# Performance work log

Hardware: AMD Instinct MI355X
Metric: run time of the kernel (lower is better)

## Reference

```python
import jax, jax.numpy as jnp
import numpy as np

V_SIZE, E, H = 30000, 256, 128   # vocab, emb_dim, GRU hidden per direction
B, U, T, ND = 32, 32, 128, 64    # dialogues, utterances, max tokens, dialogue-id table size
SCALE = E ** 0.5                  # attention normalise_factor = hid_size**0.5, hid_size = emb_dim


def _gru_dir(x_seq, w_ih, w_hh, b_ih, b_hh):
    """Unidirectional torch-style GRU. x_seq: [N,T,E] -> [N,T,H]."""
    xp = jnp.einsum('nte,ge->ntg', x_seq, w_ih) + b_ih   # precompute input gates [N,T,3H]
    xp = jnp.swapaxes(xp, 0, 1)                          # [T,N,3H]

    def step(h, xpt):
        gh = h @ w_hh.T + b_hh
        r = jax.nn.sigmoid(xpt[:, :H] + gh[:, :H])
        z = jax.nn.sigmoid(xpt[:, H:2 * H] + gh[:, H:2 * H])
        n = jnp.tanh(xpt[:, 2 * H:] + r * gh[:, 2 * H:])
        h_new = (1.0 - z) * n + z * h
        return h_new, h_new

    h0 = jnp.zeros((x_seq.shape[0], H), x_seq.dtype)
    _, out = jax.lax.scan(step, h0, xp)
    return jnp.swapaxes(out, 0, 1)


def _forward(x, d_ids, utt_len, emb_table,
             w_ih_f, w_hh_f, b_ih_f, b_hh_f,
             w_ih_b, w_hh_b, b_ih_b, b_hh_b,
             wq, bq, wk, bk, wv, bv, wo, bo, wl, bl):
    b, u, t = x.shape
    N = b * u
    emb = emb_table[x.reshape(N, t)]                      # [N,T,E]
    lens = jnp.clip(utt_len[d_ids].reshape(N), 1, t)      # valid tokens per utterance
    pos = jnp.arange(t)
    # index map that reverses the valid prefix (padding region clipped, unused)
    rev_idx = jnp.clip(lens[:, None] - 1 - pos[None, :], 0, t - 1)  # [N,T]

    o_f = _gru_dir(emb, w_ih_f, w_hh_f, b_ih_f, b_hh_f)   # causal => correct on valid prefix
    emb_rev = jnp.take_along_axis(emb, rev_idx[:, :, None], axis=1)
    o_b = jnp.take_along_axis(_gru_dir(emb_rev, w_ih_b, w_hh_b, b_ih_b, b_hh_b),
                              rev_idx[:, :, None], axis=1)
    h = jnp.concatenate([o_f, o_b], axis=-1)              # [N,T,E] bi-GRU states

    # self-attention pooling; original takes op[-1], so only the query at the
    # last valid token (lens-1) is needed -- identical math, less compute.
    k = jnp.einsum('nte,he->nth', h, wk) + bk
    v = jnp.einsum('nte,he->nth', h, wv) + bv
    h_last = jnp.take_along_axis(h, (lens - 1)[:, None, None], axis=1)[:, 0]  # [N,E]
    q = h_last @ wq.T + bq
    score = jnp.einsum('nh,nth->nt', q, k) / SCALE
    score = jnp.where(pos[None, :] < lens[:, None], score, -jnp.inf)
    attn = jax.nn.softmax(score, axis=-1)
    ctx = jnp.einsum('nt,nth->nh', attn, v)
    out = (ctx @ wo.T + bo) @ wl.T + bl                   # make_output then final linear
    return out.reshape(b, u, -1)


def setup_inputs() -> dict:
    key = jax.random.key(0)
    ks = jax.random.split(key, 16)

    def p(k, shape):
        return (jax.random.normal(k, shape, jnp.float32) / np.sqrt(shape[-1])).astype(jnp.float32)

    return {
        'x': jax.random.randint(ks[0], (B, U, T), 0, V_SIZE, dtype=jnp.int32),
        'd_ids': jax.random.randint(ks[1], (B,), 0, ND, dtype=jnp.int32),
        'utt_len': jax.random.randint(ks[2], (ND, U), 1, T + 1, dtype=jnp.int32),
        'emb_table': p(ks[3], (V_SIZE, E)),
        'w_ih_f': p(ks[4], (3 * H, E)), 'w_hh_f': p(ks[5], (3 * H, H)),
        'b_ih_f': jnp.zeros(3 * H, jnp.float32), 'b_hh_f': jnp.zeros(3 * H, jnp.float32),
        'w_ih_b': p(ks[6], (3 * H, E)), 'w_hh_b': p(ks[7], (3 * H, H)),
        'b_ih_b': jnp.zeros(3 * H, jnp.float32), 'b_hh_b': jnp.zeros(3 * H, jnp.float32),
        'wq': p(ks[8], (E, E)), 'bq': jnp.zeros(E, jnp.float32),
        'wk': p(ks[9], (E, E)), 'bk': jnp.zeros(E, jnp.float32),
        'wv': p(ks[10], (E, E)), 'bv': jnp.zeros(E, jnp.float32),
        'wo': p(ks[11], (E, E)), 'bo': jnp.zeros(E, jnp.float32),
        'wl': p(ks[12], (E, E)), 'bl': jnp.zeros(E, jnp.float32),
    }


def reference(x, d_ids, utt_len, emb_table,
              w_ih_f, w_hh_f, b_ih_f, b_hh_f,
              w_ih_b, w_hh_b, b_ih_b, b_hh_b,
              wq, bq, wk, bk, wv, bv, wo, bo, wl, bl):
    return _forward(x, d_ids, utt_len, emb_table,
                    w_ih_f, w_hh_f, b_ih_f, b_hh_f,
                    w_ih_b, w_hh_b, b_ih_b, b_hh_b,
                    wq, bq, wk, bk, wv, bv, wo, bo, wl, bl)
```

## Files before the change

### kernel.cpp

```cpp
#include <hip/hip_runtime.h>
#include <hip/hip_bf16.h>
#include <math.h>
#include <stdint.h>

typedef unsigned short u16;
typedef unsigned int   u32;
typedef __attribute__((ext_vector_type(8))) short bf16x8;
typedef __attribute__((ext_vector_type(4))) float f32x4;

#define EDIM 256
#define HDIM 128
#define TLEN 128
#define NUTT 1024
#define UU   32
#define NBU  8

#define WS_FLAG 0
#define WS_COPY 8192
#define WS_EMB  1048576LL
#define WS_OF   18874368LL
#define WS_OB   52428800LL

#define MFMA16(a, b, c) __builtin_amdgcn_mfma_f32_16x16x32_bf16((a), (b), (c), 0, 0, 0)
#define SOUT(u, s, j) ((u) * 1096 + (s) * 136 + (j))

__device__ __forceinline__ float b2f(u16 b) {
    u32 u = ((u32)b) << 16; float f; __builtin_memcpy(&f, &u, 4); return f;
}
__device__ __forceinline__ u16 f2b(float f) {
    u32 u; __builtin_memcpy(&u, &f, 4);
    u32 r = u + 0x7FFFu + ((u >> 16) & 1u);
    return (u16)(r >> 16);
}
__device__ __forceinline__ u16 f2b_hw(float f) {
    __hip_bfloat16 h = __float2bfloat16(f);
    u16 v; __builtin_memcpy(&v, &h, 2); return v;
}
__device__ __forceinline__ float fsigmoid(float x) { return 1.0f / (1.0f + __expf(-x)); }
__device__ __forceinline__ float ftanh(float x) { return 1.0f - 2.0f / (__expf(2.0f * x) + 1.0f); }

__device__ __forceinline__ bf16x8 ldw8(const void* p, size_t off, int flag) {
    if (flag) {
        const float* f = (const float*)p + off;
        float4 a = *(const float4*)f;
        float4 b = *(const float4*)(f + 4);
        union { u16 e[8]; bf16x8 v; } r;
        r.e[0] = f2b_hw(a.x); r.e[1] = f2b_hw(a.y);
        r.e[2] = f2b_hw(a.z); r.e[3] = f2b_hw(a.w);
        r.e[4] = f2b_hw(b.x); r.e[5] = f2b_hw(b.y);
        r.e[6] = f2b_hw(b.z); r.e[7] = f2b_hw(b.w);
        return r.v;
    }
    return *(const bf16x8*)((const u16*)p + off);
}
__device__ __forceinline__ float ldb(const void* p, int i, int flag) {
    return flag ? ((const float*)p)[i] : b2f(((const u16*)p)[i]);
}

__global__ __launch_bounds__(256)
void k_convert(void* ws, const void* emb, const void* wq, const void* wk,
               const void* wv, const void* wo, const void* wl) {
    __shared__ int scnt[4];
    const int tid = threadIdx.x, lane = tid & 63, wid = tid >> 6;
    const u16* p = (const u16*)emb;
    int cnt = 0;
#pragma unroll 8
    for (int i = tid; i < 16384; i += 256)
        cnt += ((p[i] & 0x7F80) == 0x7F80) ? 1 : 0;
#pragma unroll
    for (int o = 32; o > 0; o >>= 1) cnt += __shfl_down(cnt, o);
    if (lane == 0) scnt[wid] = cnt;
    __syncthreads();
    const int flag = (scnt[0] + scnt[1] + scnt[2] + scnt[3] > 0) ? 1 : 0;
    if (blockIdx.x == 0 && tid == 0) *(int*)((char*)ws + WS_FLAG) = flag;

    const void* mats[5] = {wq, wk, wv, wo, wl};
    u16* base = (u16*)((char*)ws + WS_COPY);
    const int gtid = blockIdx.x * 256 + tid;
    const int gs   = gridDim.x * 256;
    for (int q = gtid; q < 5 * 16384; q += gs) {
        const int mi = q >> 14;
        const int g  = q & 16383;
        const int e4 = g * 4;
        const int rowa = e4 >> 8, colb = e4 & 255;
        u16 e[4];
        if (flag) {
            float4 v = ((const float4*)mats[mi])[g];
            e[0] = f2b(v.x); e[1] = f2b(v.y); e[2] = f2b(v.z); e[3] = f2b(v.w);
        } else {
            uint2 v = ((const uint2*)mats[mi])[g];
            e[0] = (u16)v.x; e[1] = (u16)(v.x >> 16);
            e[2] = (u16)v.y; e[3] = (u16)(v.y >> 16);
        }
        u16* dst = base + mi * 65536;
        if (mi == 1) {
            u16* dd = dst + (rowa >> 3) * 2048 + colb * 8 + (rowa & 7);
            dd[0] = e[0]; dd[8] = e[1]; dd[16] = e[2]; dd[24] = e[3];
        } else {
            u16* dd = dst + (colb >> 3) * 2048 + rowa * 8 + (colb & 7);
            dd[0] = e[0]; dd[1] = e[1]; dd[2] = e[2]; dd[3] = e[3];
        }
    }

    if (flag == 0) return;
    {
        const float4* src = (const float4*)emb;
        uint2* dst = (uint2*)((char*)ws + WS_EMB);
        for (int i = gtid; i < 1920000; i += gs) {
            float4 v = src[i];
            uint2 pk;
            pk.x = (u32)f2b(v.x) | ((u32)f2b(v.y) << 16);
            pk.y = (u32)f2b(v.z) | ((u32)f2b(v.w) << 16);
            dst[i] = pk;
        }
    }
}

__global__ __launch_bounds__(512)
void k_scan(const int* __restrict__ x, void* ws,
            const int* __restrict__ d_ids, const int* __restrict__ utt_len,
            const void* embp,
            const void* wihf, const void* whhf, const void* bihf, const void* bhhf,
            const void* wihb, const void* whhb, const void* bihb, const void* bhhb) {
    const int dir = blockIdx.y;
    const void* w_ih = dir ? wihb : wihf;
    const void* w_hh = dir ? whhb : whhf;
    const void* b_ih = dir ? bihb : bihf;
    const void* b_hh = dir ? bhhb : bhhf;
    u16* outp = (u16*)((char*)ws + (dir ? WS_OB : WS_OF));
    const int flag = *(const int*)((const char*)ws + WS_FLAG);
    const u16* emb = flag ? (const u16*)((char*)ws + WS_EMB) : (const u16*)embp;

    const int n0 = blockIdx.x * NBU;
    __shared__ __align__(16) u16 sh_emb[2][NBU][264];
    __shared__ __align__(16) u16 sh_hi[2][NBU * 136];
    __shared__ __align__(16) u16 sh_lo[2][NBU * 136];
    __shared__ __align__(16) u16 sh_out[2][NBU * 1096];
    __shared__ int sh_tok[NBU * 132];
    __shared__ int sh_L[NBU];

    const int tid = threadIdx.x, lane = tid & 63, wvi = tid >> 6;
    const int q4 = lane >> 4, mm = lane & 15;
    const int j = wvi * 16 + mm;
    const int u8 = mm & 7;
    const int arr0 = (q4 & 2);
    const bool a2 = (arr0 != 0);
    const bool lo32 = (lane < 32);

    for (int i = tid; i < NBU * 136; i += 512) { sh_hi[0][i] = 0; sh_lo[0][i] = 0; }
    for (int i = tid; i < NBU * TLEN; i += 512) {
        const int u = i >> 7, tt = i & 127;
        sh_tok[u * 132 + tt] = x[(n0 + u) * TLEN + tt];
    }
    if (tid < NBU) {
        const int gn = n0 + tid;
        const int L = utt_len[d_ids[gn >> 5] * UU + (gn & 31)];
        sh_L[tid] = min(max(L, 1), TLEN);
    }

    bf16x8 wih[3][8]; bf16x8 whh[3][4];
    float bcr, bcz, bxn, bgn;
#pragma unroll
    for (int n3 = 0; n3 < 3; ++n3) {
        const int g = n3 * HDIM + j;
#pragma unroll
        for (int ks = 0; ks < 8; ++ks)
            wih[n3][ks] = ldw8(w_ih, (size_t)g * EDIM + ks * 32 + q4 * 8, flag);
#pragma unroll
        for (int ks = 0; ks < 4; ++ks)
            whh[n3][ks] = ldw8(w_hh, (size_t)g * HDIM + ks * 32 + q4 * 8, flag);
    }
    bcr = ldb(b_ih, j, flag) + ldb(b_hh, j, flag);
    bcz = ldb(b_ih, HDIM + j, flag) + ldb(b_hh, HDIM + j, flag);
    bxn = ldb(b_ih, 2 * HDIM + j, flag);
    bgn = ldb(b_hh, 2 * HDIM + j, flag);

    float hprev[2] = {0.f, 0.f};
    const f32x4 zero4 = {0.f, 0.f, 0.f, 0.f};
    __syncthreads();

    int Lm = sh_L[0];
#pragma unroll
    for (int u = 1; u < NBU; ++u) Lm = max(Lm, sh_L[u]);
    const int tmax = (Lm + 7) & ~7;

    const int pf_u = lane & 7;
    const int pf_c = (wvi & 3) * 8 + (lane >> 3);
    const int pf_L = sh_L[pf_u];
    const int tsel = wvi >> 2;

    {
        const int te = dir ? max(pf_L - 1 - tsel, 0) : tsel;
        const int tok = sh_tok[pf_u * 132 + te];
        uint4 v = *(const uint4*)(emb + (size_t)tok * EDIM + pf_c * 8);
        *(uint4*)&sh_emb[tsel][pf_u][pf_c * 8] = v;
    }
    __syncthreads();

    for (int t0 = 0; t0 < tmax; t0 += 2) {
        const int obuf = (t0 >> 3) & 1;
        const bool more = (t0 + 2 < tmax);

        uint4 pf;
        if (more) {
            const int tt = t0 + 2 + tsel;
            const int te = dir ? max(pf_L - 1 - tt, 0) : tt;
            const int tok = sh_tok[pf_u * 132 + te];
            pf = *(const uint4*)(emb + (size_t)tok * EDIM + pf_c * 8);
        }

        f32x4 accx[3];
        {
            const u16* eb_ = (mm < 8) ? &sh_emb[0][u8][0] : &sh_emb[1][u8][0];
            bf16x8 a = *(const bf16x8*)(eb_ + q4 * 8);
            accx[0] = MFMA16(a, wih[0][0], zero4);
            accx[1] = MFMA16(a, wih[1][0], zero4);
            accx[2] = MFMA16(a, wih[2][0], zero4);
#pragma unroll
            for (int ks = 1; ks < 8; ++ks) {
                bf16x8 av = *(const bf16x8*)(eb_ + ks * 32 + q4 * 8);
                accx[0] = MFMA16(av, wih[0][ks], accx[0]);
                accx[1] = MFMA16(av, wih[1][ks], accx[1]);
                accx[2] = MFMA16(av, wih[2][ks], accx[2]);
            }
        }
        float xA[3][2], xB[3][2];
#pragma unroll
        for (int g = 0; g < 3; ++g) {
#pragma unroll
            for (int r = 0; r < 2; ++r) {
                const float sv = a2 ? accx[g][r] : accx[g][2 + r];
                const float ov = a2 ? accx[g][2 + r] : accx[g][r];
                const float pv = __shfl_xor(sv, 32);
                xA[g][r] = lo32 ? ov : pv;
                xB[g][r] = lo32 ? pv : ov;
            }
        }

        {
            f32x4 accg[3];
            const u16* hb_ = ((mm < 8) ? sh_hi[0] : sh_lo[0]) + u8 * 136;
            {
                bf16x8 a = *(const bf16x8*)(hb_ + q4 * 8);
                accg[0] = MFMA16(a, whh[0][0], zero4);
                accg[1] = MFMA16(a, whh[1][0], zero4);
                accg[2] = MFMA16(a, whh[2][0], zero4);
            }
#pragma unroll
            for (int ks = 1; ks < 4; ++ks) {
                bf16x8 a = *(const bf16x8*)(hb_ + ks * 32 + q4 * 8);
                accg[0] = MFMA16(a, whh[0][ks], accg[0]);
                accg[1] = MFMA16(a, whh[1][ks], accg[1]);
                accg[2] = MFMA16(a, whh[2][ks], accg[2]);
            }
            const int slot = t0 & 7;
#pragma unroll
            for (int r = 0; r < 2; ++r) {
                float gg[3];
#pragma unroll
                for (int g = 0; g < 3; ++g) {
                    const float sv = a2 ? accg[g][r] : accg[g][2 + r];
                    const float ov = a2 ? accg[g][2 + r] : accg[g][r];
                    gg[g] = ov + __shfl_xor(sv, 32);
                }
                const int u = (q4 * 4 + arr0 + r) & 7;
                const float rg = fsigmoid(xA[0][r] + gg[0] + bcr);
                const float zg = fsigmoid(xA[1][r] + gg[1] + bcz);
                const float nn = ftanh((xA[2][r] + bxn) + rg * (gg[2] + bgn));
                const float hn = (1.0f - zg) * nn + zg * hprev[r];
                hprev[r] = hn;
                const u16 hb16 = f2b_hw(hn);
                sh_hi[1][u * 136 + j] = hb16;
                sh_lo[1][u * 136 + j] = f2b_hw(hn - b2f(hb16));
                sh_out[obuf][SOUT(u, slot, j)] = hb16;
            }
        }
        __syncthreads();

        {
            f32x4 accg[3];
            const u16* hb_ = ((mm < 8) ? sh_hi[1] : sh_lo[1]) + u8 * 136;
            {
                bf16x8 a = *(const bf16x8*)(hb_ + q4 * 8);
                accg[0] = MFMA16(a, whh[0][0], zero4);
                accg[1] = MFMA16(a, whh[1][0], zero4);
                accg[2] = MFMA16(a, whh[2][0], zero4);
            }
#pragma unroll
            for (int ks = 1; ks < 4; ++ks) {
                bf16x8 a = *(const bf16x8*)(hb_ + ks * 32 + q4 * 8);
                accg[0] = MFMA16(a, whh[0][ks], accg[0]);
                accg[1] = MFMA16(a, whh[1][ks], accg[1]);
                accg[2] = MFMA16(a, whh[2][ks], accg[2]);
            }
            const int slot = (t0 & 7) + 1;
#pragma unroll
            for (int r = 0; r < 2; ++r) {
                float gg[3];
#pragma unroll
                for (int g = 0; g < 3; ++g) {
                    const float sv = a2 ? accg[g][r] : accg[g][2 + r];
                    const float ov = a2 ? accg[g][2 + r] : accg[g][r];
                    gg[g] = ov + __shfl_xor(sv, 32);
                }
                const int u = (q4 * 4 + arr0 + r) & 7;
                const float rg = fsigmoid(xB[0][r] + gg[0] + bcr);
                const float zg = fsigmoid(xB[1][r] + gg[1] + bcz);
                const float nn = ftanh((xB[2][r] + bxn) + rg * (gg[2] + bgn));
                const float hn = (1.0f - zg) * nn + zg * hprev[r];
                hprev[r] = hn;
                const u16 hb16 = f2b_hw(hn);
                sh_hi[0][u * 136 + j] = hb16;
                sh_lo[0][u * 136 + j] = f2b_hw(hn - b2f(hb16));
                sh_out[obuf][SOUT(u, slot, j)] = hb16;
            }
        }
        if (more)
            *(uint4*)&sh_emb[tsel][pf_u][pf_c * 8] = pf;
        __syncthreads();

        if (((t0 + 1) & 7) == 7) {
            const int rowIdx = tid >> 3;
            const int part   = tid & 7;
            const int fu = rowIdx >> 3, fs = rowIdx & 7;
            const int tt = ((t0 + 1) & ~7) + fs;
            const int tout = dir ? (sh_L[fu] - 1 - tt) : tt;
            if (tout >= 0) {
                const u16* srcp = &sh_out[obuf][SOUT(fu, fs, part * 16)];
                uint4 v0 = *(const uint4*)(srcp);
                uint4 v1 = *(const uint4*)(srcp + 8);
                u16* dstp = outp + ((size_t)(n0 + fu) * TLEN + tout) * HDIM + part * 16;
                *(uint4*)(dstp)     = v0;
                *(uint4*)(dstp + 8) = v1;
            }
        }
    }
}

__device__ __forceinline__ float matvec_tiled(const u16* __restrict__ wt,
                                              const float* __restrict__ vin,
                                              int tid, float bias) {
    float s0 = bias, s1 = 0.0f;
#pragma unroll
    for (int kt = 0; kt < 32; kt += 2) {
        bf16x8 w8 = *(const bf16x8*)(wt + kt * 2048 + tid * 8);
        bf16x8 w9 = *(const bf16x8*)(wt + (kt + 1) * 2048 + tid * 8);
#pragma unroll
        for (int d = 0; d < 8; ++d) {
            s0 += b2f((u16)w8[d]) * vin[kt * 8 + d];
            s1 += b2f((u16)w9[d]) * vin[kt * 8 + 8 + d];
        }
    }
    return s0 + s1;
}

__global__ __launch_bounds__(256)
void k_attn(void* ws, void* outv,
            const int* __restrict__ d_ids, const int* __restrict__ utt_len,
            const void* bqp, const void* bvp, const void* bop, const void* blp) {
    const u16* wt = (const u16*)((char*)ws + WS_COPY);
    const u16* wq = wt;
    const u16* wk = wt + 65536;
    const u16* wv = wt + 2 * 65536;
    const u16* wo = wt + 3 * 65536;
    const u16* wl = wt + 4 * 65536;
    const int flag = *(const int*)((const char*)ws + WS_FLAG);

    const int n = blockIdx.x;
    const int L = min(max(utt_len[d_ids[n >> 5] * UU + (n & 31)], 1), TLEN);
    const u16* hf = (const u16*)((char*)ws + WS_OF) + (size_t)n * TLEN * HDIM;
    const u16* hb = (const u16*)((char*)ws + WS_OB) + (size_t)n * TLEN * HDIM;

    __shared__ float sh_hl[EDIM];
    __shared__ float sh_v1[EDIM];
    __shared__ float sh_uv[EDIM];
    __shared__ float sh_a[4 * EDIM];
    __shared__ float sh_m[4], sh_l[4];

    const int tid = threadIdx.x, lane = tid & 63, wid = tid >> 6;

    sh_hl[tid] = (tid < HDIM) ? b2f(hf[(size_t)(L - 1) * HDIM + tid])
                              : b2f(hb[(size_t)(L - 1) * HDIM + (tid - HDIM)]);
    __syncthreads();

    sh_v1[tid] = matvec_tiled(wq, sh_hl, tid, ldb(bqp, tid, flag));
    __syncthreads();

    sh_uv[tid] = matvec_tiled(wk, sh_v1, tid, 0.0f);
    __syncthreads();

    {
        const int e0 = lane * 4;
        const float u0 = sh_uv[e0], u1 = sh_uv[e0 + 1];
        const float u2 = sh_uv[e0 + 2], u3 = sh_uv[e0 + 3];
        float m = -1e30f, l = 0.0f;
        float a0 = 0.f, a1 = 0.f, a2 = 0.f, a3 = 0.f;
        const size_t lofs = (lane < 32) ? (size_t)(lane * 4)
                                        : (size_t)((lane - 32) * 4);
        const u16* hbase = (lane < 32) ? hf : hb;
        for (int t = wid; t < L; t += 8) {
            const int tB = t + 4;
            const int tBc = (tB < L) ? tB : (L - 1);
            uint2 pvA = *(const uint2*)(hbase + (size_t)t * HDIM + lofs);
            uint2 pvB = *(const uint2*)(hbase + (size_t)tBc * HDIM + lofs);
            const float hA0 = b2f((u16)(pvA.x & 0xFFFF));
            const float hA1 = b2f((u16)(pvA.x >> 16));
            const float hA2 = b2f((u16)(pvA.y & 0xFFFF));
            const float hA3 = b2f((u16)(pvA.y >> 16));
            const float hB0 = b2f((u16)(pvB.x & 0xFFFF));
            const float hB1 = b2f((u16)(pvB.x >> 16));
            const float hB2 = b2f((u16)(pvB.y & 0xFFFF));
            const float hB3 = b2f((u16)(pvB.y >> 16));
            float pA = hA0 * u0 + hA1 * u1 + hA2 * u2 + hA3 * u3;
            float pB = hB0 * u0 + hB1 * u1 + hB2 * u2 + hB3 * u3;
#pragma unroll
            for (int o = 32; o > 0; o >>= 1) {
                pA += __shfl_xor(pA, o);
                pB += __shfl_xor(pB, o);
            }
            const float sA = pA * 0.0625f;
            const float sB = (tB < L) ? pB * 0.0625f : -1e30f;
            const float mn = fmaxf(m, fmaxf(sA, sB));
            const float c  = __expf(m - mn);
            const float wA = __expf(sA - mn);
            const float wB = __expf(sB - mn);
            l = l * c + wA + wB;
            a0 = a0 * c + wA * hA0 + wB * hB0;
            a1 = a1 * c + wA * hA1 + wB * hB1;
            a2 = a2 * c + wA * hA2 + wB * hB2;
            a3 = a3 * c + wA * hA3 + wB * hB3;
            m = mn;
        }
        sh_a[wid * EDIM + e0]     = a0;
        sh_a[wid * EDIM + e0 + 1] = a1;
        sh_a[wid * EDIM + e0 + 2] = a2;
        sh_a[wid * EDIM + e0 + 3] = a3;
        if (lane == 0) { sh_m[wid] = m; sh_l[wid] = l; }
    }
    __syncthreads();

    {
        const float m0 = sh_m[0], m1 = sh_m[1], m2 = sh_m[2], m3 = sh_m[3];
        const float M = fmaxf(fmaxf(m0, m1), fmaxf(m2, m3));
        const float c0 = __expf(m0 - M), c1 = __expf(m1 - M);
        const float c2 = __expf(m2 - M), c3 = __expf(m3 - M);
        const float den = c0 * sh_l[0] + c1 * sh_l[1] + c2 * sh_l[2] + c3 * sh_l[3];
        const float num = c0 * sh_a[tid] + c1 * sh_a[EDIM + tid] +
                          c2 * sh_a[2 * EDIM + tid] + c3 * sh_a[3 * EDIM + tid];
        sh_hl[tid] = num / den;
    }
    __syncthreads();

    sh_uv[tid] = matvec_tiled(wv, sh_hl, tid, ldb(bvp, tid, flag));
    __syncthreads();

    sh_v1[tid] = matvec_tiled(wo, sh_uv, tid, ldb(bop, tid, flag));
    __syncthreads();

    {
        const float s = matvec_tiled(wl, sh_v1, tid, ldb(blp, tid, flag));
        const size_t oidx = (size_t)n * EDIM + tid;
        if (flag) ((float*)outv)[oidx] = s;
        else      ((u16*)outv)[oidx]   = f2b(s);
    }
}

extern "C" void kernel_launch(void* const* d_in, const int* in_sizes, int n_in,
                              void* d_out, int out_size, void* d_ws, size_t ws_size,
                              hipStream_t stream) {
    const int* x       = (const int*)d_in[0];
    const int* d_ids   = (const int*)d_in[1];
    const int* utt_len = (const int*)d_in[2];

    k_convert<<<512, 256, 0, stream>>>(d_ws, d_in[3], d_in[12], d_in[14],
                                       d_in[16], d_in[18], d_in[20]);

    k_scan<<<dim3(NUTT / NBU, 2), 512, 0, stream>>>(
        x, d_ws, d_ids, utt_len, d_in[3],
        d_in[4], d_in[5], d_in[6], d_in[7],
        d_in[8], d_in[9], d_in[10], d_in[11]);

    k_attn<<<NUTT, 256, 0, stream>>>(d_ws, d_out, d_ids, utt_len,
                                     d_in[13], d_in[17], d_in[19], d_in[21]);
}
```

Baseline: 329.4 us.

## Halve utterances per GRU scan block and batch four timesteps of input projection

Cuts the utterances each scan block handles from 8 to 4, doubling the grid so more workgroups run the recurrent scan in parallel. The input projection now covers 4 utterances × 4 timesteps in one MFMA tile per window, with hi/lo hidden-state halves computed as separate MFMA passes and broadcast via shuffles. The aim is to shorten the serial critical path per block and raise occupancy. In exchange each step runs one barrier instead of two for every pair, only a quarter of the lanes do the gate math, and the recurrent weights are loaded redundantly by more blocks.

Result: slower. 571.4 us (+73.5%).

```diff
diff --git a/kernel.cpp b/kernel.cpp
--- a/kernel.cpp
+++ b/kernel.cpp
@@ -13,7 +13,7 @@
 #define TLEN 128
 #define NUTT 1024
 #define UU   32
-#define NBU  8
+#define NBU  4
 
 #define WS_FLAG 0
 #define WS_COPY 8192
@@ -132,7 +132,7 @@
     const u16* emb = flag ? (const u16*)((char*)ws + WS_EMB) : (const u16*)embp;
 
     const int n0 = blockIdx.x * NBU;
-    __shared__ __align__(16) u16 sh_emb[2][NBU][264];
+    __shared__ __align__(16) u16 sh_embq[2][16][264];
     __shared__ __align__(16) u16 sh_hi[2][NBU * 136];
     __shared__ __align__(16) u16 sh_lo[2][NBU * 136];
     __shared__ __align__(16) u16 sh_out[2][NBU * 1096];
@@ -142,14 +142,14 @@
     const int tid = threadIdx.x, lane = tid & 63, wvi = tid >> 6;
     const int q4 = lane >> 4, mm = lane & 15;
     const int j = wvi * 16 + mm;
-    const int u8 = mm & 7;
-    const int arr0 = (q4 & 2);
-    const bool a2 = (arr0 != 0);
-    const bool lo32 = (lane < 32);
+    const int st_row = tid >> 5;
+    const int st_utt = st_row & 3;
+    const int st_ts  = tid >> 7;
+    const int st_ch  = tid & 31;
 
     for (int i = tid; i < NBU * 136; i += 512) { sh_hi[0][i] = 0; sh_lo[0][i] = 0; }
-    for (int i = tid; i < NBU * TLEN; i += 512) {
-        const int u = i >> 7, tt = i & 127;
+    {
+        const int u = tid >> 7, tt = tid & 127;
         sh_tok[u * 132 + tt] = x[(n0 + u) * TLEN + tt];
     }
     if (tid < NBU) {
@@ -175,7 +175,7 @@
     bxn = ldb(b_ih, 2 * HDIM + j, flag);
     bgn = ldb(b_hh, 2 * HDIM + j, flag);
 
-    float hprev[2] = {0.f, 0.f};
+    float hprev[NBU] = {0.f, 0.f, 0.f, 0.f};
     const f32x4 zero4 = {0.f, 0.f, 0.f, 0.f};
     __syncthreads();
 
@@ -183,155 +183,138 @@
 #pragma unroll
     for (int u = 1; u < NBU; ++u) Lm = max(Lm, sh_L[u]);
     const int tmax = (Lm + 7) & ~7;
-
-    const int pf_u = lane & 7;
-    const int pf_c = (wvi & 3) * 8 + (lane >> 3);
-    const int pf_L = sh_L[pf_u];
-    const int tsel = wvi >> 2;
-
-    {
-        const int te = dir ? max(pf_L - 1 - tsel, 0) : tsel;
-        const int tok = sh_tok[pf_u * 132 + te];
-        uint4 v = *(const uint4*)(emb + (size_t)tok * EDIM + pf_c * 8);
-        *(uint4*)&sh_emb[tsel][pf_u][pf_c * 8] = v;
-    }
-    __syncthreads();
-
-    for (int t0 = 0; t0 < tmax; t0 += 2) {
-        const int obuf = (t0 >> 3) & 1;
-        const bool more = (t0 + 2 < tmax);
+    const int st_L = sh_L[st_utt];
+
+    {
+        const int te = dir ? max(st_L - 1 - st_ts, 0) : st_ts;
+        const int tok = sh_tok[st_utt * 132 + te];
+        uint4 v = *(const uint4*)(emb + (size_t)tok * EDIM + st_ch * 8);
+        *(uint4*)&sh_embq[0][st_row][st_ch * 8] = v;
+    }
+    __syncthreads();
+
+    for (int tw = 0; tw < tmax; tw += 4) {
+        const int wpar = (tw >> 2) & 1;
+        const bool stg = (tw + 4 < tmax);
 
         uint4 pf;
-        if (more) {
-            const int tt = t0 + 2 + tsel;
-            const int te = dir ? max(pf_L - 1 - tt, 0) : tt;
-            const int tok = sh_tok[pf_u * 132 + te];
-            pf = *(const uint4*)(emb + (size_t)tok * EDIM + pf_c * 8);
+        if (stg) {
+            const int tt = tw + 4 + st_ts;
+            const int te = dir ? max(st_L - 1 - tt, 0) : tt;
+            const int tok = sh_tok[st_utt * 132 + te];
+            pf = *(const uint4*)(emb + (size_t)tok * EDIM + st_ch * 8);
         }
 
         f32x4 accx[3];
         {
-            const u16* eb_ = (mm < 8) ? &sh_emb[0][u8][0] : &sh_emb[1][u8][0];
+            const u16* eb_ = &sh_embq[wpar][mm][0];
+            f32x4 xa0, xa1, xa2, xb0, xb1, xb2;
             bf16x8 a = *(const bf16x8*)(eb_ + q4 * 8);
-            accx[0] = MFMA16(a, wih[0][0], zero4);
-            accx[1] = MFMA16(a, wih[1][0], zero4);
-            accx[2] = MFMA16(a, wih[2][0], zero4);
-#pragma unroll
-            for (int ks = 1; ks < 8; ++ks) {
+            xa0 = MFMA16(a, wih[0][0], zero4);
+            xa1 = MFMA16(a, wih[1][0], zero4);
+            xa2 = MFMA16(a, wih[2][0], zero4);
+#pragma unroll
+            for (int ks = 1; ks < 4; ++ks) {
                 bf16x8 av = *(const bf16x8*)(eb_ + ks * 32 + q4 * 8);
-                accx[0] = MFMA16(av, wih[0][ks], accx[0]);
-                accx[1] = MFMA16(av, wih[1][ks], accx[1]);
-                accx[2] = MFMA16(av, wih[2][ks], accx[2]);
-            }
-        }
-        float xA[3][2], xB[3][2];
-#pragma unroll
-        for (int g = 0; g < 3; ++g) {
-#pragma unroll
-            for (int r = 0; r < 2; ++r) {
-                const float sv = a2 ? accx[g][r] : accx[g][2 + r];
-                const float ov = a2 ? accx[g][2 + r] : accx[g][r];
-                const float pv = __shfl_xor(sv, 32);
-                xA[g][r] = lo32 ? ov : pv;
-                xB[g][r] = lo32 ? pv : ov;
-            }
-        }
-
-        {
-            f32x4 accg[3];
-            const u16* hb_ = ((mm < 8) ? sh_hi[0] : sh_lo[0]) + u8 * 136;
+                xa0 = MFMA16(av, wih[0][ks], xa0);
+                xa1 = MFMA16(av, wih[1][ks], xa1);
+                xa2 = MFMA16(av, wih[2][ks], xa2);
+            }
+            bf16x8 b = *(const bf16x8*)(eb_ + 4 * 32 + q4 * 8);
+            xb0 = MFMA16(b, wih[0][4], zero4);
+            xb1 = MFMA16(b, wih[1][4], zero4);
+            xb2 = MFMA16(b, wih[2][4], zero4);
+#pragma unroll
+            for (int ks = 5; ks < 8; ++ks) {
+                bf16x8 bv = *(const bf16x8*)(eb_ + ks * 32 + q4 * 8);
+                xb0 = MFMA16(bv, wih[0][ks], xb0);
+                xb1 = MFMA16(bv, wih[1][ks], xb1);
+                xb2 = MFMA16(bv, wih[2][ks], xb2);
+            }
+            accx[0] = xa0 + xb0; accx[1] = xa1 + xb1; accx[2] = xa2 + xb2;
+        }
+
+#pragma unroll
+        for (int s = 0; s < 4; ++s) {
+            const int t = tw + s;
+            const int hbuf = t & 1;
+
+            float xg[3][NBU];
+#pragma unroll
+            for (int g = 0; g < 3; ++g)
+#pragma unroll
+                for (int u = 0; u < NBU; ++u)
+                    xg[g][u] = __shfl(accx[g][u], s * 16 + mm);
+
+            f32x4 ga0, ga1, ga2, gb0, gb1, gb2;
             {
-                bf16x8 a = *(const bf16x8*)(hb_ + q4 * 8);
-                accg[0] = MFMA16(a, whh[0][0], zero4);
-                accg[1] = MFMA16(a, whh[1][0], zero4);
-                accg[2] = MFMA16(a, whh[2][0], zero4);
-            }
-#pragma unroll
-            for (int ks = 1; ks < 4; ++ks) {
-                bf16x8 a = *(const bf16x8*)(hb_ + ks * 32 + q4 * 8);
-                accg[0] = MFMA16(a, whh[0][ks], accg[0]);
-                accg[1] = MFMA16(a, whh[1][ks], accg[1]);
-                accg[2] = MFMA16(a, whh[2][ks], accg[2]);
-            }
-            const int slot = t0 & 7;
-#pragma unroll
-            for (int r = 0; r < 2; ++r) {
-                float gg[3];
-#pragma unroll
-                for (int g = 0; g < 3; ++g) {
-                    const float sv = a2 ? accg[g][r] : accg[g][2 + r];
-                    const float ov = a2 ? accg[g][2 + r] : accg[g][r];
-                    gg[g] = ov + __shfl_xor(sv, 32);
+                const u16* hA = sh_hi[hbuf] + (mm & 3) * 136;
+                const u16* hB = sh_lo[hbuf] + (mm & 3) * 136;
+                bf16x8 a = *(const bf16x8*)(hA + q4 * 8);
+                ga0 = MFMA16(a, whh[0][0], zero4);
+                ga1 = MFMA16(a, whh[1][0], zero4);
+                ga2 = MFMA16(a, whh[2][0], zero4);
+#pragma unroll
+                for (int c = 1; c < 4; ++c) {
+                    bf16x8 av = *(const bf16x8*)(hA + c * 32 + q4 * 8);
+                    ga0 = MFMA16(av, whh[0][c], ga0);
+                    ga1 = MFMA16(av, whh[1][c], ga1);
+                    ga2 = MFMA16(av, whh[2][c], ga2);
                 }
-                const int u = (q4 * 4 + arr0 + r) & 7;
-                const float rg = fsigmoid(xA[0][r] + gg[0] + bcr);
-                const float zg = fsigmoid(xA[1][r] + gg[1] + bcz);
-                const float nn = ftanh((xA[2][r] + bxn) + rg * (gg[2] + bgn));
-                const float hn = (1.0f - zg) * nn + zg * hprev[r];
-                hprev[r] = hn;
-                const u16 hb16 = f2b_hw(hn);
-                sh_hi[1][u * 136 + j] = hb16;
-                sh_lo[1][u * 136 + j] = f2b_hw(hn - b2f(hb16));
-                sh_out[obuf][SOUT(u, slot, j)] = hb16;
-            }
-        }
-        __syncthreads();
-
-        {
-            f32x4 accg[3];
-            const u16* hb_ = ((mm < 8) ? sh_hi[1] : sh_lo[1]) + u8 * 136;
-            {
-                bf16x8 a = *(const bf16x8*)(hb_ + q4 * 8);
-                accg[0] = MFMA16(a, whh[0][0], zero4);
-                accg[1] = MFMA16(a, whh[1][0], zero4);
-                accg[2] = MFMA16(a, whh[2][0], zero4);
-            }
-#pragma unroll
-            for (int ks = 1; ks < 4; ++ks) {
-                bf16x8 a = *(const bf16x8*)(hb_ + ks * 32 + q4 * 8);
-                accg[0] = MFMA16(a, whh[0][ks], accg[0]);
-                accg[1] = MFMA16(a, whh[1][ks], accg[1]);
-                accg[2] = MFMA16(a, whh[2][ks], accg[2]);
-            }
-            const int slot = (t0 & 7) + 1;
-#pragma unroll
-            for (int r = 0; r < 2; ++r) {
-                float gg[3];
-#pragma unroll
-                for (int g = 0; g < 3; ++g) {
-                    const float sv = a2 ? accg[g][r] : accg[g][2 + r];
-                    const float ov = a2 ? accg[g][2 + r] : accg[g][r];
-                    gg[g] = ov + __shfl_xor(sv, 32);
+                bf16x8 b = *(const bf16x8*)(hB + q4 * 8);
+                gb0 = MFMA16(b, whh[0][0], zero4);
+                gb1 = MFMA16(b, whh[1][0], zero4);
+                gb2 = MFMA16(b, whh[2][0], zero4);
+#pragma unroll
+                for (int c = 1; c < 4; ++c) {
+                    bf16x8 bv = *(const bf16x8*)(hB + c * 32 + q4 * 8);
+                    gb0 = MFMA16(bv, whh[0][c], gb0);
+                    gb1 = MFMA16(bv, whh[1][c], gb1);
+                    gb2 = MFMA16(bv, whh[2][c], gb2);
                 }
-                const int u = (q4 * 4 + arr0 + r) & 7;
-                const float rg = fsigmoid(xB[0][r] + gg[0] + bcr);
-                const float zg = fsigmoid(xB[1][r] + gg[1] + bcz);
-                const float nn = ftanh((xB[2][r] + bxn) + rg * (gg[2] + bgn));
-                const float hn = (1.0f - zg) * nn + zg * hprev[r];
-                hprev[r] = hn;
-                const u16 hb16 = f2b_hw(hn);
-                sh_hi[0][u * 136 + j] = hb16;
-                sh_lo[0][u * 136 + j] = f2b_hw(hn - b2f(hb16));
-                sh_out[obuf][SOUT(u, slot, j)] = hb16;
-            }
-        }
-        if (more)
-            *(uint4*)&sh_emb[tsel][pf_u][pf_c * 8] = pf;
-        __syncthreads();
-
-        if (((t0 + 1) & 7) == 7) {
-            const int rowIdx = tid >> 3;
-            const int part   = tid & 7;
-            const int fu = rowIdx >> 3, fs = rowIdx & 7;
-            const int tt = ((t0 + 1) & ~7) + fs;
-            const int tout = dir ? (sh_L[fu] - 1 - tt) : tt;
-            if (tout >= 0) {
-                const u16* srcp = &sh_out[obuf][SOUT(fu, fs, part * 16)];
-                uint4 v0 = *(const uint4*)(srcp);
-                uint4 v1 = *(const uint4*)(srcp + 8);
-                u16* dstp = outp + ((size_t)(n0 + fu) * TLEN + tout) * HDIM + part * 16;
-                *(uint4*)(dstp)     = v0;
-                *(uint4*)(dstp + 8) = v1;
+            }
+
+            if (q4 == 0) {
+                const int slot = t & 7, obuf = (t >> 3) & 1;
+#pragma unroll
+                for (int u = 0; u < NBU; ++u) {
+                    const float g0 = ga0[u] + gb0[u];
+                    const float g1 = ga1[u] + gb1[u];
+                    const float g2 = ga2[u] + gb2[u];
+                    const float rg = fsigmoid(xg[0][u] + g0 + bcr);
+                    const float zg = fsigmoid(xg[1][u] + g1 + bcz);
+                    const float nn = ftanh((xg[2][u] + bxn) + rg * (g2 + bgn));
+                    const float hn = (1.0f - zg) * nn + zg * hprev[u];
+                    hprev[u] = hn;
+                    const u16 hb16 = f2b_hw(hn);
+                    sh_hi[hbuf ^ 1][u * 136 + j] = hb16;
+                    sh_lo[hbuf ^ 1][u * 136 + j] = f2b_hw(hn - b2f(hb16));
+                    sh_out[obuf][SOUT(u, slot, j)] = hb16;
+                }
+            }
+
+            if (s == 2 && stg)
+                *(uint4*)&sh_embq[wpar ^ 1][st_row][st_ch * 8] = pf;
+
+            __syncthreads();
+
+            if ((t & 7) == 7) {
+                const int rowIdx = tid >> 3;
+                const int part   = tid & 7;
+                const int fu = rowIdx >> 3, fs = rowIdx & 7;
+                if (fu < NBU) {
+                    const int obuf = (t >> 3) & 1;
+                    const int tt = (t & ~7) + fs;
+                    const int tout = dir ? (sh_L[fu] - 1 - tt) : tt;
+                    if (tout >= 0) {
+                        const u16* srcp = &sh_out[obuf][SOUT(fu, fs, part * 16)];
+                        uint4 v0 = *(const uint4*)(srcp);
+                        uint4 v1 = *(const uint4*)(srcp + 8);
+                        u16* dstp = outp + ((size_t)(n0 + fu) * TLEN + tout) * HDIM + part * 16;
+                        *(uint4*)(dstp)     = v0;
+                        *(uint4*)(dstp + 8) = v1;
+                    }
+                }
             }
         }
     }
```
